# Optimization experiments

Measured on AMD Instinct MI355X. Metric: run time of the kernel, lower is better.

Reference implementation:

```python
import jax, jax.numpy as jnp
import numpy as np
from jax import lax

B = 2
IMG = 640.0
MIN_LEVEL, MAX_LEVEL = 3, 7
NUM_CLASSES = 91          # includes background (index 0)
MAX_TOTAL = 100
IOU_THR = 0.3
SCORE_THR = 0.05
PRE_NMS = 5000
BBOX_CLIP = float(np.log(1000.0 / 16.0))  # standard box-transform clip


def _level_anchors(level):
    """RetinaNet-style anchors for one pyramid level, [H*W*9, 4] in (y1,x1,y2,x2)."""
    stride = 2 ** level
    feat = int(IMG) // stride
    cy = (np.arange(feat, dtype=np.float32) + 0.5) * stride
    cx = (np.arange(feat, dtype=np.float32) + 0.5) * stride
    cy, cx = np.meshgrid(cy, cx, indexing='ij')
    base = 4.0 * stride
    anchors = []
    for octave in (2 ** 0.0, 2 ** (1.0 / 3.0), 2 ** (2.0 / 3.0)):
        for ar in (0.5, 1.0, 2.0):
            h = base * octave * np.sqrt(ar)
            w = base * octave / np.sqrt(ar)
            anchors.append(np.stack([cy - h / 2, cx - w / 2, cy + h / 2, cx + w / 2], -1))
    a = np.stack(anchors, -2).reshape(-1, 4)
    return a.astype(np.float32)


def setup_inputs():
    key = jax.random.key(0)
    inp = {}
    for level in range(MIN_LEVEL, MAX_LEVEL + 1):
        anc = _level_anchors(level)
        n = anc.shape[0]
        key, kb, kc = jax.random.split(key, 3)
        inp[f'box_outputs_{level}'] = 0.2 * jax.random.normal(kb, (B, n, 4), jnp.float32)
        inp[f'class_outputs_{level}'] = jax.random.normal(kc, (B, n, NUM_CLASSES), jnp.float32) - 2.0
        inp[f'anchor_boxes_{level}'] = jnp.broadcast_to(jnp.asarray(anc)[None], (B, n, 4))
    inp['image_shape'] = jnp.full((B, 2), IMG, jnp.float32)
    return inp


def _decode_boxes(enc, anchors):
    # faithful to box_utils.decode_boxes (with the +1/-1 pixel convention)
    dy, dx = enc[..., 0], enc[..., 1]
    dh = jnp.minimum(enc[..., 2], BBOX_CLIP)
    dw = jnp.minimum(enc[..., 3], BBOX_CLIP)
    ah = anchors[..., 2] - anchors[..., 0] + 1.0
    aw = anchors[..., 3] - anchors[..., 1] + 1.0
    ayc = anchors[..., 0] + 0.5 * ah
    axc = anchors[..., 1] + 0.5 * aw
    yc = dy * ah + ayc
    xc = dx * aw + axc
    h = jnp.exp(dh) * ah
    w = jnp.exp(dw) * aw
    ymin = yc - 0.5 * h
    xmin = xc - 0.5 * w
    return jnp.stack([ymin, xmin, ymin + h - 1.0, xmin + w - 1.0], axis=-1)


def _clip_boxes(boxes, image_shape):
    h = image_shape[:, 0:1]
    w = image_shape[:, 1:2]
    max_len = jnp.stack([h, w, h, w], axis=-1)  # [B,1,4]
    return jnp.clip(boxes, 0.0, max_len)


def _greedy_nms(scores, boxes):
    """Sorted greedy NMS over one (batch, class) lane.
    scores: [K] sorted descending (filtered entries are -1), boxes: [K,4].
    Returns top MAX_TOTAL selected (score, box) in descending score order,
    padded with score=-1 / zero boxes (matches sorted_non_max_suppression_padded).
    """
    areas = (boxes[:, 2] - boxes[:, 0]) * (boxes[:, 3] - boxes[:, 1])

    def step(active, _):
        masked = jnp.where(active, scores, -jnp.inf)
        i = jnp.argmax(masked)
        s = masked[i]
        valid = s > -1.0
        b = boxes[i]
        yy1 = jnp.maximum(b[0], boxes[:, 0])
        xx1 = jnp.maximum(b[1], boxes[:, 1])
        yy2 = jnp.minimum(b[2], boxes[:, 2])
        xx2 = jnp.minimum(b[3], boxes[:, 3])
        inter = jnp.maximum(yy2 - yy1, 0.0) * jnp.maximum(xx2 - xx1, 0.0)
        iou = inter / ((b[2] - b[0]) * (b[3] - b[1]) + areas - inter + 1e-8)
        active = active & (iou <= IOU_THR)
        active = active.at[i].set(False)
        out_s = jnp.where(valid, s, -1.0)
        out_b = jnp.where(valid, b, jnp.zeros_like(b))
        return active, (out_s, out_b)

    _, (sel_s, sel_b) = lax.scan(step, jnp.ones(scores.shape[0], bool), None, length=MAX_TOTAL)
    return sel_s, sel_b


def reference(box_outputs_3, box_outputs_4, box_outputs_5, box_outputs_6, box_outputs_7,
              class_outputs_3, class_outputs_4, class_outputs_5, class_outputs_6, class_outputs_7,
              anchor_boxes_3, anchor_boxes_4, anchor_boxes_5, anchor_boxes_6, anchor_boxes_7,
              image_shape):
    box_list = [box_outputs_3, box_outputs_4, box_outputs_5, box_outputs_6, box_outputs_7]
    cls_list = [class_outputs_3, class_outputs_4, class_outputs_5, class_outputs_6, class_outputs_7]
    anc_list = [anchor_boxes_3, anchor_boxes_4, anchor_boxes_5, anchor_boxes_6, anchor_boxes_7]

    boxes, scores = [], []
    for bo, co, an in zip(box_list, cls_list, anc_list):
        scores.append(jax.nn.sigmoid(co)[..., 1:])            # drop background class 0
        boxes.append(_clip_boxes(_decode_boxes(bo, an), image_shape))
    boxes = jnp.concatenate(boxes, axis=1)                     # [B,N,4] class-agnostic
    scores = jnp.concatenate(scores, axis=1)                   # [B,N,C]

    scores_t = jnp.transpose(scores, (0, 2, 1))                # [B,C,N]
    k = min(scores_t.shape[-1], PRE_NMS)
    top_s, idx = lax.top_k(scores_t, k)                        # [B,C,K]
    top_b = jax.vmap(lambda b, i: b[i])(boxes, idx)            # [B,C,K,4]

    # filter_boxes_by_scores: score -> -1, boxes -> 0 below threshold
    mask = top_s >= SCORE_THR
    top_s = jnp.where(mask, top_s, -1.0)
    top_b = top_b * mask[..., None].astype(top_b.dtype)

    sel_s, sel_b = jax.vmap(jax.vmap(_greedy_nms))(top_s, top_b)  # [B,C,T], [B,C,T,4]
    Bsz, C, T = sel_s.shape
    classes = jnp.broadcast_to(jnp.arange(C, dtype=jnp.int32)[None, :, None], (Bsz, C, T))

    flat_s = sel_s.reshape(Bsz, C * T)
    flat_b = sel_b.reshape(Bsz, C * T, 4)
    flat_c = classes.reshape(Bsz, C * T)

    final_s, fidx = lax.top_k(flat_s, MAX_TOTAL)
    final_b = jnp.take_along_axis(flat_b, fidx[..., None], axis=1)
    final_c = jnp.take_along_axis(flat_c, fidx, axis=1) + 1    # nmsed_classes += 1
    valid = jnp.sum((final_s > -1.0).astype(jnp.int32), axis=1)
    return final_b, final_s, final_c, valid
```

## Files before the change

kernel.cpp:

```cpp
#include <hip/hip_runtime.h>
#include <hip/hip_bf16.h>

typedef unsigned long long u64;
typedef unsigned int u32;

#define A_TOTAL 76725
#define NCLS 90
#define KTOP 5000u
#define MAXT 100
#define KTHR 0x3D4CCCCDu
#define TCAP 2048u
#define SCAP 512u
#define NSEL 384u

__device__ __forceinline__ u64 pack_key(u32 k, u32 i) {
  return ((u64)k << 32) | (u64)(0xFFFFFFFFu - i);
}

__device__ __forceinline__ int dig05(u64 k) {
  float s = __uint_as_float((u32)(k >> 32));
  int d = (int)((s - 0.5f) * 8175.0f);
  return min(max(d, 0), 4095);
}

__device__ __forceinline__ void cut4096w(const u32* hh, u32 need, int wl,
                                         u32& B, u32& incl, u32& above, u32& total) {
  int lo = wl << 6;
  u32 s = 0;
  #pragma unroll
  for (int j = 0; j < 64; ++j) s += hh[lo + j];
  u32 suf = s;
  #pragma unroll
  for (int off = 1; off < 64; off <<= 1) {
    u32 v = __shfl_down(suf, off, 64);
    if (wl < 64 - off) suf += v;
  }
  total = __shfl(suf, 0, 64);
  if (total < need) { B = 0; incl = total; above = 0; return; }
  u32 sufnext = suf - s;
  bool cross = (suf >= need) && (sufnext < need);
  u64 bal = __ballot(cross);
  int gl = (int)__ffsll((unsigned long long)bal) - 1;
  int glo = gl << 6;
  u32 aboveG = __shfl(sufnext, gl, 64);
  u32 hb = hh[glo + wl];
  u32 sufb = hb;
  #pragma unroll
  for (int off = 1; off < 64; off <<= 1) {
    u32 v = __shfl_down(sufb, off, 64);
    if (wl < 64 - off) sufb += v;
  }
  bool c2 = (aboveG + sufb >= need) && (aboveG + sufb - hb < need);
  u64 bal2 = __ballot(c2);
  int jB = (int)__ffsll((unsigned long long)bal2) - 1;
  B = (u32)(glo + jB);
  incl = aboveG + __shfl(sufb, jB, 64);
  above = incl - __shfl(hb, jB, 64);
}

__device__ __forceinline__ void bitonic_desc(u64* a, u32 n, int tid, int nth) {
  u32 P = 2; while (P < n) P <<= 1;
  for (u32 i = tid; i < P; i += nth) if (i >= n) a[i] = 0ULL;
  __syncthreads();
  for (u32 kk = 2; kk <= P; kk <<= 1) {
    for (u32 jj = kk >> 1; jj; jj >>= 1) {
      for (u32 i = tid; i < P; i += nth) {
        u32 ixj = i ^ jj;
        if (ixj > i) {
          u64 x = a[i], y = a[ixj];
          bool up = ((i & kk) == 0);
          if (up ? (x < y) : (x > y)) { a[i] = y; a[ixj] = x; }
        }
      }
      __syncthreads();
    }
  }
}

__device__ __forceinline__ int bitset_scan(const u64* key_s, const float4* boxes4, size_t bbase,
                                           int C, float4* wbox, float4* bbox,
                                           float* outS, float* outB, int w, int wl) {
  int cur = 0;
  while (w < MAXT && cur < C) {
    int p = cur + wl;
    bool valid = (p < C);
    u64 kk = valid ? key_s[p] : 0ull;
    float4 mybox = make_float4(-3e30f, -3e30f, -3e30f, -3e30f);
    if (valid) {
      u32 idx = 0xFFFFFFFFu - (u32)(kk & 0xFFFFFFFFull);
      mybox = boxes4[bbase + idx];
    }
    bbox[wl] = mybox;
    float myarea = (mybox.z - mybox.x) * (mybox.w - mybox.y);
    bool alive = valid;
    for (int j = 0; j < w; ++j) {
      float4 pb = wbox[j];
      float yy1 = fmaxf(pb.x, mybox.x), xx1 = fmaxf(pb.y, mybox.y);
      float yy2 = fminf(pb.z, mybox.z), xx2 = fminf(pb.w, mybox.w);
      float inter = fmaxf(yy2 - yy1, 0.0f) * fmaxf(xx2 - xx1, 0.0f);
      bool bad = false;
      if (inter > 0.0f) {
        float pa = (pb.z - pb.x) * (pb.w - pb.y);
        bad = inter / (pa + myarea - inter + 1e-8f) > 0.3f;
      }
      alive = alive && !bad;
    }
    u64 krow = 0ull;
    int jmax = C - cur; if (jmax > 64) jmax = 64;
    for (int j = 0; j < jmax; ++j) {
      float4 pb = bbox[j];
      float yy1 = fmaxf(pb.x, mybox.x), xx1 = fmaxf(pb.y, mybox.y);
      float yy2 = fminf(pb.z, mybox.z), xx2 = fminf(pb.w, mybox.w);
      float inter = fmaxf(yy2 - yy1, 0.0f) * fmaxf(xx2 - xx1, 0.0f);
      bool kill = false;
      if (inter > 0.0f) {
        float pa = (pb.z - pb.x) * (pb.w - pb.y);
        kill = inter / (pa + myarea - inter + 1e-8f) > 0.3f;
      }
      if (kill) krow |= (1ull << j);
    }
    u32 krlo = (u32)krow, krhi = (u32)(krow >> 32);
    u64 amask = __ballot(alive);
    int myord = -1;
    while (amask != 0ull && w < MAXT) {
      int js = (int)__ffsll((unsigned long long)amask) - 1;
      u32 klo = __shfl(krlo, js, 64);
      u32 khi = __shfl(krhi, js, 64);
      u64 kr = ((u64)khi << 32) | (u64)klo;
      if (wl == js) myord = w;
      amask &= ~kr;
      amask &= ~(1ull << js);
      w++;
    }
    if (myord >= 0) {
      outS[myord] = __uint_as_float((u32)(kk >> 32));
      *(float4*)(outB + myord * 4) = mybox;
      wbox[myord] = mybox;
    }
    cur += 64;
  }
  return w;
}

__device__ __forceinline__ int lazy_scan_g(const u64* key_s, const float4* boxes4, size_t bbase,
                                           int C, float4* wbox, float* outS, float* outB,
                                           int w, int wl) {
  int cur = 0;
  while (w < MAXT && cur < C) {
    int p = cur + wl;
    bool alive = (p < C);
    u64 kk = alive ? key_s[p] : 0ull;
    float4 mybox = make_float4(0.f, 0.f, 0.f, 0.f);
    if (alive) {
      u32 idx = 0xFFFFFFFFu - (u32)(kk & 0xFFFFFFFFull);
      mybox = boxes4[bbase + idx];
    }
    float myarea = (mybox.z - mybox.x) * (mybox.w - mybox.y);
    for (int j = 0; j < w; ++j) {
      float4 pb = wbox[j];
      float yy1 = fmaxf(pb.x, mybox.x), xx1 = fmaxf(pb.y, mybox.y);
      float yy2 = fminf(pb.z, mybox.z), xx2 = fminf(pb.w, mybox.w);
      float inter = fmaxf(yy2 - yy1, 0.0f) * fmaxf(xx2 - xx1, 0.0f);
      bool bad = false;
      if (inter > 0.0f) {
        float pa = (pb.z - pb.x) * (pb.w - pb.y);
        bad = inter / (pa + myarea - inter + 1e-8f) > 0.3f;
      }
      alive = alive && !bad;
    }
    for (;;) {
      u64 bal = __ballot(alive);
      if (bal == 0ull) break;
      int js = (int)__ffsll((unsigned long long)bal) - 1;
      float4 pb;
      pb.x = __shfl(mybox.x, js, 64);
      pb.y = __shfl(mybox.y, js, 64);
      pb.z = __shfl(mybox.z, js, 64);
      pb.w = __shfl(mybox.w, js, 64);
      u64 wk = __shfl(kk, js, 64);
      if (wl == 0) {
        outS[w] = __uint_as_float((u32)(wk >> 32));
        *(float4*)(outB + w * 4) = pb;
        wbox[w] = pb;
      }
      w++;
      if (w >= MAXT) break;
      if (wl <= js) alive = false;
      else if (alive) {
        float yy1 = fmaxf(pb.x, mybox.x), xx1 = fmaxf(pb.y, mybox.y);
        float yy2 = fminf(pb.z, mybox.z), xx2 = fminf(pb.w, mybox.w);
        float inter = fmaxf(yy2 - yy1, 0.0f) * fmaxf(xx2 - xx1, 0.0f);
        if (inter > 0.0f) {
          float pa = (pb.z - pb.x) * (pb.w - pb.y);
          if (inter / (pa + myarea - inter + 1e-8f) > 0.3f) alive = false;
        }
      }
    }
    cur += 64;
  }
  return w;
}

__global__ __launch_bounds__(256) void zero_kernel(u32* __restrict__ p, int n) {
  int i = blockIdx.x * 256 + threadIdx.x;
  if (i < n) p[i] = 0;
}

__device__ __forceinline__ void coll_elem(int i, float x, int b, int base, int slice,
                                          u64* __restrict__ listT_g, u32* __restrict__ cnt_pad) {
  if (x >= 0.0f) {
    u32 a = (u32)i / 91u;
    u32 c = (u32)i - a * 91u;
    if (c != 0u) {
      float s = 1.0f / (1.0f + expf(-x));
      int lane = b * NCLS + (int)c - 1;
      u32 idx = (u32)base + a;
      u32 p = atomicAdd(&cnt_pad[lane * 128 + slice * 16], 1u);
      if (p < SCAP) listT_g[(((size_t)lane * 8 + slice) << 9) + p] = pack_key(__float_as_uint(s), idx);
    }
  }
}

__global__ __launch_bounds__(256) void front_kernel(
    const float* __restrict__ bx0, const float* __restrict__ bx1, const float* __restrict__ bx2,
    const float* __restrict__ bx3, const float* __restrict__ bx4,
    const float* __restrict__ an0, const float* __restrict__ an1, const float* __restrict__ an2,
    const float* __restrict__ an3, const float* __restrict__ an4,
    const float* __restrict__ c3, const float* __restrict__ c4, const float* __restrict__ c5,
    const float* __restrict__ c6, const float* __restrict__ c7,
    const float* __restrict__ img, float* __restrict__ boxes,
    u64* __restrict__ listT_g, u32* __restrict__ cnt_pad)
{
  int blk = blockIdx.x, tid = threadIdx.x;
  if (blk < 600) {
    int t = blk * 256 + tid;
    if (t >= 2 * A_TOTAL) return;
    int b = t / A_TOTAL, a = t % A_TOTAL;
    const float* bp; const float* ap; int al; int nl;
    if (a < 57600)      { bp = bx0; ap = an0; al = a;          nl = 57600; }
    else if (a < 72000) { bp = bx1; ap = an1; al = a - 57600;  nl = 14400; }
    else if (a < 75600) { bp = bx2; ap = an2; al = a - 72000;  nl = 3600;  }
    else if (a < 76500) { bp = bx3; ap = an3; al = a - 75600;  nl = 900;   }
    else                { bp = bx4; ap = an4; al = a - 76500;  nl = 225;   }
    float4 e  = *(const float4*)(bp + ((size_t)b * nl + al) * 4);
    float4 an = *(const float4*)(ap + ((size_t)b * nl + al) * 4);
    const float CLIP = 4.135166556742356f;
    float ah  = an.z - an.x + 1.0f;
    float aw  = an.w - an.y + 1.0f;
    float ayc = an.x + 0.5f * ah;
    float axc = an.y + 0.5f * aw;
    float dh = fminf(e.z, CLIP), dw = fminf(e.w, CLIP);
    float yc = e.x * ah + ayc;
    float xc = e.y * aw + axc;
    float h  = expf(dh) * ah;
    float w  = expf(dw) * aw;
    float ymin = yc - 0.5f * h;
    float xmin = xc - 0.5f * w;
    float ymax = ymin + h - 1.0f;
    float xmax = xmin + w - 1.0f;
    float H = img[b * 2 + 0], W = img[b * 2 + 1];
    float4 o;
    o.x = fminf(fmaxf(ymin, 0.0f), H);
    o.y = fminf(fmaxf(xmin, 0.0f), W);
    o.z = fminf(fmaxf(ymax, 0.0f), H);
    o.w = fminf(fmaxf(xmax, 0.0f), W);
    *(float4*)(boxes + (size_t)t * 4) = o;
    return;
  }
  int blk2 = blk - 600;
  int slice = blk2 & 7;
  const float* cls; int n, base, b, loc, J, lvl;
  if (blk2 < 2560)      { lvl = 0; cls = c3; n = 57600; base = 0;     J = 1280; int r = blk2;        b = r >= J; loc = b ? r - J : r; }
  else if (blk2 < 3200) { lvl = 1; cls = c4; n = 14400; base = 57600; J = 320;  int r = blk2 - 2560; b = r >= J; loc = b ? r - J : r; }
  else if (blk2 < 3360) { lvl = 2; cls = c5; n = 3600;  base = 72000; J = 80;   int r = blk2 - 3200; b = r >= J; loc = b ? r - J : r; }
  else if (blk2 < 3400) { lvl = 3; cls = c6; n = 900;   base = 75600; J = 20;   int r = blk2 - 3360; b = r >= J; loc = b ? r - J : r; }
  else                  { lvl = 4; cls = c7; n = 225;   base = 76500; J = 10;   int r = blk2 - 3400; b = r >= J; loc = b ? r - J : r; }

  if (lvl <= 3) {
    int F4 = n * 91 / 4;
    int chunk = (F4 + J - 1) / J;
    int q0 = loc * chunk;
    int q1 = q0 + chunk; if (q1 > F4) q1 = F4;
    const float4* src4 = (const float4*)(cls + (size_t)b * n * 91);
    for (int q = q0 + tid; q < q1; q += 256) {
      float4 v = src4[q];
      int i0 = q << 2;
      coll_elem(i0,     v.x, b, base, slice, listT_g, cnt_pad);
      coll_elem(i0 + 1, v.y, b, base, slice, listT_g, cnt_pad);
      coll_elem(i0 + 2, v.z, b, base, slice, listT_g, cnt_pad);
      coll_elem(i0 + 3, v.w, b, base, slice, listT_g, cnt_pad);
    }
  } else {
    int F = n * 91;
    int chunk = (F + J - 1) / J;
    int s0 = loc * chunk;
    int s1 = s0 + chunk; if (s1 > F) s1 = F;
    const float* src = cls + (size_t)b * F;
    for (int i = s0 + tid; i < s1; i += 256) coll_elem(i, src[i], b, base, slice, listT_g, cnt_pad);
  }
}

__global__ __launch_bounds__(256) void nms_kernel(
    const float* __restrict__ c3, const float* __restrict__ c4, const float* __restrict__ c5,
    const float* __restrict__ c6, const float* __restrict__ c7,
    const float* __restrict__ boxes, const u64* __restrict__ listT_g,
    const u32* __restrict__ cnt_pad, float* __restrict__ nms_s, float* __restrict__ nms_b)
{
  __shared__ __align__(16) char big[40960];
  __shared__ __align__(16) u64 listE[2048];
  __shared__ u64 key_s[2048];
  __shared__ __align__(16) u32 histL[4096];
  __shared__ float4 wbox[MAXT];
  __shared__ float4 bbox[64];
  __shared__ u32 wtot[4];
  __shared__ u32 sh_flag, sh_mid, sh_bigS, sh_cS;
  __shared__ u64 sh_minPrev;
  __shared__ u32 sh_w, sh_done, sh_eidx, sh_Rthr, sh_eSorted, sh_bigF;
  __shared__ u32 sh_B, sh_incl, sh_above, sh_total, sh_cA, sh_cE, sh_B2;

  int tid = threadIdx.x;
  int lane = blockIdx.x;
  int b = lane / NCLS, c = lane % NCLS;
  const float4* boxes4 = (const float4*)boxes;
  size_t bbase = (size_t)b * A_TOTAL;
  const u64 thrpack = ((u64)KTHR) << 32;

  float* outS = nms_s + (size_t)lane * MAXT;
  float* outB = nms_b + (size_t)lane * MAXT * 4;

  u32 pre[9]; pre[0] = 0;
  bool of = false;
  #pragma unroll
  for (int j = 0; j < 8; ++j) {
    u32 cj = cnt_pad[lane * 128 + j * 16];
    of |= (cj > SCAP);
    pre[j + 1] = pre[j] + cj;
  }
  u32 cnt = pre[8];
  if (tid == 0) { sh_flag = (of || cnt > TCAP) ? 1u : 0u; sh_mid = 0; sh_bigS = 0; }
  __syncthreads();

  if (!sh_flag) {
    u64 kr[8];
    #pragma unroll
    for (int r = 0; r < 8; ++r) {
      u32 s = (u32)tid + (u32)r * 256u;
      u64 k = 0ull;
      if (s < cnt) {
        u32 j = 0;
        #pragma unroll
        for (int t = 1; t < 8; ++t) if (s >= pre[t]) j = (u32)t;
        k = listT_g[(((size_t)lane * 8 + j) << 9) + (s - pre[j])];
      }
      kr[r] = k;
    }

    for (int i = tid; i < 4096; i += 256) histL[i] = 0;
    __syncthreads();
    #pragma unroll
    for (int r = 0; r < 8; ++r) if (kr[r]) atomicAdd(&histL[dig05(kr[r])], 1u);
    __syncthreads();
    if (tid < 64) {
      u32 Bx, ix, ax, tx;
      cut4096w(histL, NSEL, tid, Bx, ix, ax, tx);
      if (tid == 0) { sh_B = Bx; sh_incl = ix; sh_total = tx; sh_cS = 0; }
    }
    __syncthreads();
    u32 B = sh_B, incl = sh_incl, total = sh_total;
    bool selAll = (total < NSEL);
    u32 Csel = selAll ? total : incl;
    if (Csel <= 768u) {
      u64* sel = (u64*)histL;
      #pragma unroll
      for (int r = 0; r < 8; ++r) {
        u64 k = kr[r];
        if (k && (selAll || (u32)dig05(k) >= B)) {
          u32 p = atomicAdd(&sh_cS, 1u);
          if (p < 768u) sel[p] = k;
        }
      }
      __syncthreads();
      u32 Cs = sh_cS; if (Cs > 768u) Cs = 768u;
      for (u32 j = tid; j < Cs; j += 256) {
        u64 kj = sel[j];
        u32 rk = 0;
        for (u32 i2 = 0; i2 < Cs; ++i2) rk += (sel[i2] > kj) ? 1u : 0u;
        key_s[rk] = kj;
      }
      __syncthreads();
      if (tid < 64) {
        int w = bitset_scan(key_s, boxes4, bbase, (int)Cs, wbox, bbox, outS, outB, 0, tid);
        if (tid == 0) {
          sh_w = (u32)w;
          if (w < MAXT) { if (selAll) sh_flag = 1; else sh_mid = 1; }
        }
      }
    } else {
      if (tid == 0) sh_mid = 1;
    }
    __syncthreads();

    if (sh_mid && !sh_flag) {
      for (int i = tid; i < 4096; i += 256) histL[i] = 0;
      if (tid == 0) sh_bigS = 0;
      __syncthreads();
      #pragma unroll
      for (int r = 0; r < 8; ++r) if (kr[r]) atomicAdd(&histL[dig05(kr[r])], 1u);
      __syncthreads();
      {
        int t0 = tid << 4;
        u32 hloc[16]; u32 ssum = 0;
        #pragma unroll
        for (int j = 0; j < 16; ++j) { hloc[j] = histL[t0 + j]; ssum += hloc[j]; }
        int wl = tid & 63, wid = tid >> 6;
        u32 suf = ssum;
        #pragma unroll
        for (int off = 1; off < 64; off <<= 1) {
          u32 v = __shfl_down(suf, off, 64);
          if (wl < 64 - off) suf += v;
        }
        if (wl == 0) wtot[wid] = suf;
        __syncthreads();
        u32 cross = 0;
        for (int w2 = wid + 1; w2 < 4; ++w2) cross += wtot[w2];
        u32 run = (suf - ssum) + cross;
        #pragma unroll
        for (int j = 15; j >= 0; --j) { u32 b2 = run; run += hloc[j]; histL[t0 + j] = b2; }
      }
      __syncthreads();
      #pragma unroll
      for (int r = 0; r < 8; ++r) {
        u64 k = kr[r];
        if (k) {
          u32 pos = atomicAdd(&histL[dig05(k)], 1u);
          if (pos < TCAP) key_s[pos] = k;
        }
      }
      __syncthreads();
      {
        int t0 = tid << 4;
        for (int j = 0; j < 16; ++j) {
          u32 d = (u32)(t0 + j);
          u32 end = histL[d];
          u32 start = (d == 4095u) ? 0u : histL[d + 1];
          u32 cc = end - start;
          if (cc >= 2u) {
            if (cc <= 48u) {
              for (u32 a2 = start + 1; a2 < end; ++a2) {
                u64 kv = key_s[a2];
                int bi = (int)a2 - 1;
                while (bi >= (int)start && key_s[bi] < kv) { key_s[bi + 1] = key_s[bi]; --bi; }
                key_s[bi + 1] = kv;
              }
            } else sh_bigS = 1;
          }
        }
      }
      __syncthreads();
      if (sh_bigS) bitonic_desc(key_s, cnt, tid, 256);
      if (tid < 64) {
        int w = bitset_scan(key_s, boxes4, bbase, (int)cnt, wbox, bbox, outS, outB, 0, tid);
        if (tid == 0) {
          sh_w = (u32)w;
          if (w < MAXT) sh_flag = 1;
        }
      }
    }
  }
  __syncthreads();
  if (!sh_flag) {
    u32 w = sh_w;
    for (u32 p = w + (u32)tid; p < MAXT; p += 256) {
      outS[p] = -1.0f;
      *(float4*)(outB + p * 4) = make_float4(0.f, 0.f, 0.f, 0.f);
    }
    return;
  }

  auto sb_of = [&](int i) -> u32 {
    const float* p; int al, nl;
    if (i < 57600)      { p = c3; al = i;          nl = 57600; }
    else if (i < 72000) { p = c4; al = i - 57600;  nl = 14400; }
    else if (i < 75600) { p = c5; al = i - 72000;  nl = 3600;  }
    else if (i < 76500) { p = c6; al = i - 75600;  nl = 900;   }
    else                { p = c7; al = i - 76500;  nl = 225;   }
    float x = p[((size_t)b * nl + al) * 91 + (c + 1)];
    float s = 1.0f / (1.0f + expf(-x));
    return __float_as_uint(s);
  };

  u64* listA = (u64*)big;
  for (int i = tid; i < 4096; i += 256) histL[i] = 0;
  if (tid == 0) {
    sh_cA = 0; sh_cE = 0; sh_w = 0; sh_done = 0; sh_eidx = 0; sh_eSorted = 0; sh_minPrev = ~0ull;
  }
  __syncthreads();
  for (int i = tid; i < A_TOTAL; i += 256) atomicAdd(&histL[sb_of(i) >> 19], 1u);
  __syncthreads();
  if (tid < 64) {
    u32 Bx, ix, ax, tx;
    cut4096w(histL, KTOP, tid, Bx, ix, ax, tx);
    if (tid == 0) sh_B = Bx;
  }
  __syncthreads();
  u32 B = sh_B;
  for (int i = tid; i < A_TOTAL; i += 256) {
    u32 u = sb_of(i);
    u32 bkt = u >> 19;
    if (bkt > B) {
      u32 p = atomicAdd(&sh_cA, 1u);
      if (p < 5120u) listA[p] = pack_key(u, (u32)i);
    } else if (bkt == B) {
      u32 p = atomicAdd(&sh_cE, 1u);
      if (p < 2048u) listE[p] = pack_key(u, (u32)i);
    }
  }
  __syncthreads();
  u32 g = sh_cA, h = sh_cE;
  if (h > 2048u) {
    for (int i = tid; i < 4096; i += 256) histL[i] = 0;
    if (tid == 0) sh_cE = 0;
    __syncthreads();
    for (int i = tid; i < A_TOTAL; i += 256) {
      u32 u = sb_of(i);
      if ((u >> 19) == B) atomicAdd(&histL[(u >> 7) & 0xFFFu], 1u);
    }
    __syncthreads();
    u32 R1 = KTOP - g;
    if (tid < 64) {
      u32 Bx, ix, ax, tx;
      cut4096w(histL, R1, tid, Bx, ix, ax, tx);
      if (tid == 0) sh_B2 = Bx;
    }
    __syncthreads();
    u32 B2 = sh_B2;
    for (int i = tid; i < A_TOTAL; i += 256) {
      u32 u = sb_of(i);
      if ((u >> 19) == B) {
        u32 sb2 = (u >> 7) & 0xFFFu;
        if (sb2 > B2) {
          u32 p = atomicAdd(&sh_cA, 1u);
          if (p < 5120u) listA[p] = pack_key(u, (u32)i);
        } else if (sb2 == B2) {
          u32 p = atomicAdd(&sh_cE, 1u);
          if (p < 2048u) listE[p] = pack_key(u, (u32)i);
        }
      }
    }
    __syncthreads();
    g = sh_cA; h = sh_cE; if (h > 2048u) h = 2048u;
  }
  if (g > 5120u) g = 5120u;
  u32 R = (g < KTOP) ? (KTOP - g) : 0u; if (R > h) R = h;

  u64 ak[20];
  #pragma unroll
  for (int r = 0; r < 20; ++r) {
    u32 s2 = (u32)tid + (u32)r * 256u;
    u64 kp = (s2 < g) ? listA[s2] : 0ull;
    if (kp < thrpack) kp = 0ull;
    ak[r] = kp;
  }
  __syncthreads();
  u32* cntArr = (u32*)big;

  const float LO0  = 0.04f;
  const float INV0 = 4096.0f / (1.001f - 0.04f);

  for (int seg = 0; seg < 7200; ++seg) {
    __syncthreads();
    if (sh_w >= MAXT || sh_done) break;
    u64 minPrev = sh_minPrev;

    int digLvl = 0;
    u32 A_B0 = 0, A_B1 = 0;
    float lo1 = 0.f, inv1 = 0.f;
    u64 kMask = 0, kPref = 0;
    int m1shift = 32;
    int selMode = -1;
    u32 selB = 0;
    u32 C = 0;
    bool fromE = false;

    for (int lvl = 0; lvl < 8; ++lvl) {
      for (int i = tid; i < 4096; i += 256) histL[i] = 0;
      __syncthreads();
      #pragma unroll
      for (int r = 0; r < 20; ++r) {
        u64 k = ak[r];
        if (!k || k >= minPrev) continue;
        float s = __uint_as_float((u32)(k >> 32));
        if (digLvl >= 1) { int d0 = (int)((s - LO0) * INV0); d0 = min(max(d0, 0), 4095); if ((u32)d0 != A_B0) continue; }
        if (digLvl >= 2) { int d1 = (int)((s - lo1) * inv1); d1 = min(max(d1, 0), 4095); if ((u32)d1 != A_B1) continue; }
        if (digLvl >= 3 && ((k & kMask) != kPref)) continue;
        u32 d;
        if (digLvl == 0)      { int t0 = (int)((s - LO0) * INV0); d = (u32)min(max(t0, 0), 4095); }
        else if (digLvl == 1) { int t1 = (int)((s - lo1) * inv1); d = (u32)min(max(t1, 0), 4095); }
        else                  d = (u32)((k >> m1shift) & 0xFFFull);
        atomicAdd(&histL[d], 1u);
      }
      __syncthreads();
      if (tid < 64) {
        u32 Bx, ix, ax, tx;
        cut4096w(histL, 1024u, tid, Bx, ix, ax, tx);
        if (tid == 0) { sh_B = Bx; sh_incl = ix; sh_above = ax; sh_total = tx; }
      }
      __syncthreads();
      u32 total = sh_total, incl = sh_incl, above = sh_above, Bx = sh_B;
      if (total == 0u)   { fromE = true; break; }
      if (total < 1024u) { selMode = 0; C = total; break; }
      if (incl <= 2048u) { selMode = 1; selB = Bx; C = incl; break; }
      if (above > 0u)    { selMode = 2; selB = Bx; C = above; break; }
      if (digLvl == 0) {
        A_B0 = Bx;
        lo1 = LO0 + (float)Bx / INV0;
        inv1 = INV0 * 4096.0f;
        digLvl = 1;
      } else if (digLvl == 1) {
        A_B1 = Bx;
        digLvl = 2; m1shift = 32;
      } else {
        kPref |= ((u64)Bx << m1shift);
        kMask |= (0xFFFull << m1shift);
        m1shift -= 12;
        digLvl++;
      }
      __syncthreads();
    }

    if (fromE) {
      if (!sh_eSorted) {
        bitonic_desc(listE, h, tid, 256);
        if (tid == 0) {
          u32 lo = 0, hi2 = h;
          while (lo < hi2) { u32 mid = (lo + hi2) >> 1; if (listE[mid] >= thrpack) lo = mid + 1; else hi2 = mid; }
          sh_Rthr = (R < lo) ? R : lo;
          sh_eSorted = 1;
        }
        __syncthreads();
      }
      u32 eidx = sh_eidx;
      u32 take = (sh_Rthr > eidx) ? (sh_Rthr - eidx) : 0u;
      if (take > 2048u) take = 2048u;
      if (take == 0u) { if (tid == 0) sh_done = 1; continue; }
      for (u32 i = tid; i < take; i += 256) key_s[i] = listE[eidx + i];
      C = take;
      if (tid == 0) sh_eidx = eidx + take;
    } else {
      u32 hloc[16];
      {
        int t0 = tid << 4;
        u32 ssum = 0;
        #pragma unroll
        for (int j = 0; j < 16; ++j) { hloc[j] = histL[t0 + j]; ssum += hloc[j]; }
        int wl = tid & 63, wid = tid >> 6;
        u32 suf = ssum;
        #pragma unroll
        for (int off = 1; off < 64; off <<= 1) {
          u32 v = __shfl_down(suf, off, 64);
          if (wl < 64 - off) suf += v;
        }
        if (wl == 0) wtot[wid] = suf;
        __syncthreads();
        u32 cross = 0;
        for (int w2 = wid + 1; w2 < 4; ++w2) cross += wtot[w2];
        u32 run = (suf - ssum) + cross;
        #pragma unroll
        for (int j = 15; j >= 0; --j) { u32 base2 = run; run += hloc[j]; histL[t0 + j] = base2; }
      }
      for (int i = tid; i < 4096; i += 256) cntArr[i] = 0;
      if (tid == 0) sh_bigF = 0;
      __syncthreads();
      #pragma unroll
      for (int r = 0; r < 20; ++r) {
        u64 k = ak[r];
        if (!k || k >= minPrev) continue;
        float s = __uint_as_float((u32)(k >> 32));
        if (digLvl >= 1) { int d0 = (int)((s - LO0) * INV0); d0 = min(max(d0, 0), 4095); if ((u32)d0 != A_B0) continue; }
        if (digLvl >= 2) { int d1 = (int)((s - lo1) * inv1); d1 = min(max(d1, 0), 4095); if ((u32)d1 != A_B1) continue; }
        if (digLvl >= 3 && ((k & kMask) != kPref)) continue;
        u32 d;
        if (digLvl == 0)      { int t0x = (int)((s - LO0) * INV0); d = (u32)min(max(t0x, 0), 4095); }
        else if (digLvl == 1) { int t1x = (int)((s - lo1) * inv1); d = (u32)min(max(t1x, 0), 4095); }
        else                  d = (u32)((k >> m1shift) & 0xFFFull);
        if (selMode == 1)      { if (d < selB) continue; }
        else if (selMode == 2) { if (d <= selB) continue; }
        u32 pos = histL[d] + atomicAdd(&cntArr[d], 1u);
        if (pos < 2048u) key_s[pos] = k;
      }
      __syncthreads();
      {
        int t0 = tid << 4;
        for (int j = 0; j < 16; ++j) {
          u32 bkt = (u32)(t0 + j);
          u32 cc = cntArr[bkt];
          if (cc >= 2u) {
            if (cc <= 48u) {
              u32 basep = histL[bkt];
              for (u32 a2 = 1; a2 < cc; ++a2) {
                u64 kv = key_s[basep + a2];
                int bi = (int)a2 - 1;
                while (bi >= 0 && key_s[basep + bi] < kv) { key_s[basep + bi + 1] = key_s[basep + bi]; --bi; }
                key_s[basep + bi + 1] = kv;
              }
            } else sh_bigF = 1;
          }
        }
      }
      __syncthreads();
      if (sh_bigF) bitonic_desc(key_s, C, tid, 256);
      if (tid == 0) sh_minPrev = key_s[C - 1];
    }
    __syncthreads();

    if (tid < 64) {
      int w = lazy_scan_g(key_s, boxes4, bbase, (int)C, wbox, outS, outB, (int)sh_w, tid);
      if (tid == 0) sh_w = (u32)w;
    }
  }

  __syncthreads();
  u32 w = sh_w;
  for (u32 p = w + (u32)tid; p < MAXT; p += 256) {
    outS[p] = -1.0f;
    *(float4*)(outB + p * 4) = make_float4(0.f, 0.f, 0.f, 0.f);
  }
}

__global__ __launch_bounds__(256) void merge_kernel(
    const float* __restrict__ nms_s, const float* __restrict__ nms_b,
    float* __restrict__ out_b, float* __restrict__ out_s,
    float* __restrict__ out_c, float* __restrict__ out_v)
{
  __shared__ u64 keys[NCLS * MAXT];
  __shared__ u32 hist[4096];
  __shared__ u64 sel[640];
  __shared__ u32 sh_cnt, sh_valid;
  __shared__ u32 sh_B, sh_incl, sh_above, sh_total;

  int b = blockIdx.x, tid = threadIdx.x;
  const int NTOT = NCLS * MAXT;

  for (int i = tid; i < NTOT; i += 256) {
    float s = nms_s[(size_t)b * NTOT + i];
    u32 u = __float_as_uint(s);
    u = (u & 0x80000000u) ? ~u : (u | 0x80000000u);
    keys[i] = ((u64)u << 32) | (u64)(0xFFFFFFFFu - (u32)i);
  }
  if (tid == 0) { sh_cnt = 0; sh_valid = 0; }

  u64 prefVal = 0;
  u64 T = 0;
  u32 need = MAXT;
  const int shifts[6] = {52, 40, 28, 16, 4, 0};
  const int widths[6] = {12, 12, 12, 12, 12, 4};
  for (int lvl = 0; lvl < 6; ++lvl) {
    int s = shifts[lvl], w = widths[lvl];
    for (int i = tid; i < 4096; i += 256) hist[i] = 0;
    __syncthreads();
    u32 dmask = (1u << w) - 1u;
    for (int i = tid; i < NTOT; i += 256) {
      u64 k = keys[i];
      if (lvl > 0 && (k >> (s + w)) != (prefVal >> (s + w))) continue;
      atomicAdd(&hist[(u32)((k >> s) & dmask)], 1u);
    }
    __syncthreads();
    if (tid < 64) {
      u32 Bx, ix, ax, tx;
      cut4096w(hist, need, tid, Bx, ix, ax, tx);
      if (tid == 0) { sh_B = Bx; sh_incl = ix; sh_above = ax; sh_total = tx; }
    }
    __syncthreads();
    u32 B = sh_B, incl = sh_incl, above = sh_above;
    if (incl <= 512u || lvl == 5) {
      T = prefVal | ((u64)B << s);
      break;
    }
    prefVal |= ((u64)B << s);
    need -= above;
  }
  __syncthreads();

  for (int i = tid; i < NTOT; i += 256) {
    u64 k = keys[i];
    if (k >= T) {
      u32 p = atomicAdd(&sh_cnt, 1u);
      if (p < 640u) sel[p] = k;
    }
  }
  __syncthreads();
  u32 cnt = sh_cnt; if (cnt > 640u) cnt = 640u;

  for (u32 j = tid; j < cnt; j += 256) {
    u64 kj = sel[j];
    u32 r = 0;
    for (u32 i = 0; i < cnt; ++i) r += (sel[i] > kj) ? 1u : 0u;
    if (r < (u32)MAXT) {
      u32 u = (u32)(kj >> 32);
      u32 bits = (u & 0x80000000u) ? (u ^ 0x80000000u) : ~u;
      float sc = __uint_as_float(bits);
      u32 flat = 0xFFFFFFFFu - (u32)(kj & 0xFFFFFFFFull);
      int cls = (int)(flat / MAXT), pos = (int)(flat % MAXT);
      out_s[b * MAXT + r] = sc;
      out_c[b * MAXT + r] = (float)(cls + 1);
      *(float4*)(out_b + ((size_t)b * MAXT + r) * 4) =
          *(const float4*)(nms_b + (((size_t)b * NCLS + cls) * MAXT + pos) * 4);
      if (sc > -1.0f) atomicAdd(&sh_valid, 1u);
    }
  }
  __syncthreads();
  if (tid == 0) out_v[b] = (float)sh_valid;
}

extern "C" void kernel_launch(void* const* d_in, const int* in_sizes, int n_in,
                              void* d_out, int out_size, void* d_ws, size_t ws_size,
                              hipStream_t stream)
{
  const float* box[5]; const float* cls[5]; const float* anc[5];
  bool interleaved = (in_sizes[1] == 2 * 57600 * 91);
  if (interleaved) {
    for (int l = 0; l < 5; ++l) {
      box[l] = (const float*)d_in[3 * l + 0];
      cls[l] = (const float*)d_in[3 * l + 1];
      anc[l] = (const float*)d_in[3 * l + 2];
    }
  } else {
    for (int l = 0; l < 5; ++l) {
      box[l] = (const float*)d_in[l];
      cls[l] = (const float*)d_in[5 + l];
      anc[l] = (const float*)d_in[10 + l];
    }
  }
  const float* img = (const float*)d_in[15];

  float* ws = (float*)d_ws;
  float* boxes_ws = ws;
  u32*   cnt_pad  = (u32*)(boxes_ws + 613800);
  u64*   listT_g  = (u64*)(cnt_pad + 180 * 128);
  float* nms_s    = (float*)(listT_g + 180 * 8 * 512);
  float* nms_b    = nms_s + 18000;

  const int NZ = 180 * 128;
  zero_kernel<<<(NZ + 255) / 256, 256, 0, stream>>>(cnt_pad, NZ);

  front_kernel<<<4020, 256, 0, stream>>>(
      box[0], box[1], box[2], box[3], box[4],
      anc[0], anc[1], anc[2], anc[3], anc[4],
      cls[0], cls[1], cls[2], cls[3], cls[4],
      img, boxes_ws, listT_g, cnt_pad);

  nms_kernel<<<180, 256, 0, stream>>>(cls[0], cls[1], cls[2], cls[3], cls[4],
                                      boxes_ws, listT_g, cnt_pad, nms_s, nms_b);

  float* out_b = (float*)d_out;
  float* out_s = out_b + 800;
  float* out_c = out_s + 200;
  float* out_v = out_c + 200;
  merge_kernel<<<2, 256, 0, stream>>>(nms_s, nms_b, out_b, out_s, out_c, out_v);
}
```

Baseline: 117.9 us.

## Derive a global score lower bound from per-class top-8 NMS survivors to prune candidates

Adds two kernels. The first runs a tiny NMS over each class's top-8 keys. The second finds the 100th-largest survivor score per batch, which is a lower bound on the final top-100 threshold. The NMS kernel now keeps only keys at or above that bound, replacing the histogram cut and the mid-path radix/bitonic sort. If more than SELCAP keys remain, or on panic, it falls back to the generic path. This costs two extra launches, including a single-block serial kernel, plus global reads in exchange for much smaller per-class sorts.

```diff
diff --git a/kernel.cpp b/kernel.cpp
--- a/kernel.cpp
+++ b/kernel.cpp
@@ -11,16 +11,10 @@
 #define KTHR 0x3D4CCCCDu
 #define TCAP 2048u
 #define SCAP 512u
-#define NSEL 384u
+#define SELCAP 512u
 
 __device__ __forceinline__ u64 pack_key(u32 k, u32 i) {
   return ((u64)k << 32) | (u64)(0xFFFFFFFFu - i);
-}
-
-__device__ __forceinline__ int dig05(u64 k) {
-  float s = __uint_as_float((u32)(k >> 32));
-  int d = (int)((s - 0.5f) * 8175.0f);
-  return min(max(d, 0), 4095);
 }
 
 __device__ __forceinline__ void cut4096w(const u32* hh, u32 need, int wl,
@@ -300,11 +294,151 @@
   }
 }
 
+__global__ __launch_bounds__(256) void top8_kernel(
+    const u64* __restrict__ listT_g, const u32* __restrict__ cnt_pad,
+    const float* __restrict__ boxes, u32* __restrict__ win8, u32* __restrict__ w8cnt)
+{
+  __shared__ u64 wred[4];
+  __shared__ u64 sh_top;
+  __shared__ u64 topk[8];
+  __shared__ float4 tb[8];
+  int tid = threadIdx.x;
+  int lane = blockIdx.x;
+
+  u32 pre[9]; pre[0] = 0;
+  bool of = false;
+  #pragma unroll
+  for (int j = 0; j < 8; ++j) {
+    u32 cj = cnt_pad[lane * 128 + j * 16];
+    of |= (cj > SCAP);
+    pre[j + 1] = pre[j] + cj;
+  }
+  u32 cnt = pre[8];
+  if (of || cnt > TCAP) { if (tid == 0) w8cnt[lane] = 0xFFFFu; return; }
+
+  u64 kr[8];
+  #pragma unroll
+  for (int r = 0; r < 8; ++r) {
+    u32 s = (u32)tid + (u32)r * 256u;
+    u64 k = 0ull;
+    if (s < cnt) {
+      u32 j = 0;
+      #pragma unroll
+      for (int t = 1; t < 8; ++t) if (s >= pre[t]) j = (u32)t;
+      k = listT_g[(((size_t)lane * 8 + j) << 9) + (s - pre[j])];
+    }
+    kr[r] = k;
+  }
+
+  int nt = 0;
+  for (int it = 0; it < 8; ++it) {
+    u64 m = kr[0];
+    #pragma unroll
+    for (int r = 1; r < 8; ++r) if (kr[r] > m) m = kr[r];
+    #pragma unroll
+    for (int off = 1; off < 64; off <<= 1) {
+      u64 o = __shfl_xor(m, off);
+      if (o > m) m = o;
+    }
+    if ((tid & 63) == 0) wred[tid >> 6] = m;
+    __syncthreads();
+    if (tid == 0) {
+      u64 w = wred[0];
+      if (wred[1] > w) w = wred[1];
+      if (wred[2] > w) w = wred[2];
+      if (wred[3] > w) w = wred[3];
+      sh_top = w;
+      topk[it] = w;
+    }
+    __syncthreads();
+    u64 ch = sh_top;
+    if (ch == 0ull) break;
+    #pragma unroll
+    for (int r = 0; r < 8; ++r) if (kr[r] == ch) kr[r] = 0ull;
+    nt = it + 1;
+  }
+  __syncthreads();
+  const float4* boxes4 = (const float4*)boxes;
+  size_t bbase = (size_t)(lane / NCLS) * A_TOTAL;
+  if (tid < nt) {
+    u32 idx = 0xFFFFFFFFu - (u32)(topk[tid] & 0xFFFFFFFFull);
+    tb[tid] = boxes4[bbase + idx];
+  }
+  __syncthreads();
+  if (tid == 0) {
+    float4 abox[8];
+    int w8 = 0;
+    for (int i = 0; i < nt; ++i) {
+      float4 mb = tb[i];
+      float ma = (mb.z - mb.x) * (mb.w - mb.y);
+      bool alive = true;
+      for (int j = 0; j < w8; ++j) {
+        float4 pb = abox[j];
+        float yy1 = fmaxf(pb.x, mb.x), xx1 = fmaxf(pb.y, mb.y);
+        float yy2 = fminf(pb.z, mb.z), xx2 = fminf(pb.w, mb.w);
+        float inter = fmaxf(yy2 - yy1, 0.0f) * fmaxf(xx2 - xx1, 0.0f);
+        if (inter > 0.0f) {
+          float pa = (pb.z - pb.x) * (pb.w - pb.y);
+          if (inter / (pa + ma - inter + 1e-8f) > 0.3f) alive = false;
+        }
+      }
+      if (alive) {
+        win8[lane * 8 + w8] = (u32)(topk[i] >> 32);
+        abox[w8] = mb;
+        w8++;
+      }
+    }
+    w8cnt[lane] = (u32)w8;
+  }
+}
+
+__global__ __launch_bounds__(256) void tlb2_kernel(const u32* __restrict__ win8,
+                                                   const u32* __restrict__ w8cnt,
+                                                   u32* __restrict__ tparams)
+{
+  __shared__ u32 vals[720];
+  __shared__ u32 sh_T, sh_tot, sh_panic;
+  int t = threadIdx.x;
+  if (t == 0) sh_panic = 0;
+  __syncthreads();
+  for (int b = 0; b < 2; ++b) {
+    if (t == 0) { sh_T = 0xFFFFFFFFu; sh_tot = 0; }
+    __syncthreads();
+    u32 mycnt = 0;
+    for (int i = t; i < 720; i += 256) {
+      int ln = b * NCLS + i / 8;
+      u32 cc = w8cnt[ln];
+      u32 v = 0;
+      if (cc == 0xFFFFu) { sh_panic = 1; }
+      else if ((u32)(i & 7) < cc) { v = win8[ln * 8 + (i & 7)]; mycnt++; }
+      vals[i] = v;
+    }
+    atomicAdd(&sh_tot, mycnt);
+    __syncthreads();
+    for (int i = t; i < 720; i += 256) {
+      u32 v = vals[i];
+      if (v) {
+        u32 r = 0;
+        for (int j = 0; j < 720; ++j) r += (vals[j] > v) ? 1u : 0u;
+        if (r <= 99u) atomicMin(&sh_T, v);
+      }
+    }
+    __syncthreads();
+    if (t == 0) {
+      tparams[b] = sh_T;
+      if (sh_tot < 100u || sh_T == 0xFFFFFFFFu) sh_panic = 1;
+    }
+    __syncthreads();
+  }
+  if (t == 0) tparams[2] = sh_panic;
+}
+
 __global__ __launch_bounds__(256) void nms_kernel(
     const float* __restrict__ c3, const float* __restrict__ c4, const float* __restrict__ c5,
     const float* __restrict__ c6, const float* __restrict__ c7,
     const float* __restrict__ boxes, const u64* __restrict__ listT_g,
-    const u32* __restrict__ cnt_pad, float* __restrict__ nms_s, float* __restrict__ nms_b)
+    const u32* __restrict__ cnt_pad, const u32* __restrict__ tparams,
+    float* __restrict__ nms_s, float* __restrict__ nms_b)
 {
   __shared__ __align__(16) char big[40960];
   __shared__ __align__(16) u64 listE[2048];
@@ -313,7 +447,7 @@
   __shared__ float4 wbox[MAXT];
   __shared__ float4 bbox[64];
   __shared__ u32 wtot[4];
-  __shared__ u32 sh_flag, sh_mid, sh_bigS, sh_cS;
+  __shared__ u32 sh_flag, sh_cS;
   __shared__ u64 sh_minPrev;
   __shared__ u32 sh_w, sh_done, sh_eidx, sh_Rthr, sh_eSorted, sh_bigF;
   __shared__ u32 sh_B, sh_incl, sh_above, sh_total, sh_cA, sh_cE, sh_B2;
@@ -337,50 +471,32 @@
     pre[j + 1] = pre[j] + cj;
   }
   u32 cnt = pre[8];
-  if (tid == 0) { sh_flag = (of || cnt > TCAP) ? 1u : 0u; sh_mid = 0; sh_bigS = 0; }
+  u32 Tlb = tparams[b], panic = tparams[2];
+  if (tid == 0) { sh_flag = (of || cnt > TCAP || panic) ? 1u : 0u; sh_cS = 0; }
   __syncthreads();
 
   if (!sh_flag) {
-    u64 kr[8];
+    const u64 Tpack = ((u64)Tlb) << 32;
+    u64* sel = (u64*)histL;
     #pragma unroll
     for (int r = 0; r < 8; ++r) {
       u32 s = (u32)tid + (u32)r * 256u;
-      u64 k = 0ull;
       if (s < cnt) {
         u32 j = 0;
         #pragma unroll
         for (int t = 1; t < 8; ++t) if (s >= pre[t]) j = (u32)t;
-        k = listT_g[(((size_t)lane * 8 + j) << 9) + (s - pre[j])];
-      }
-      kr[r] = k;
-    }
-
-    for (int i = tid; i < 4096; i += 256) histL[i] = 0;
-    __syncthreads();
-    #pragma unroll
-    for (int r = 0; r < 8; ++r) if (kr[r]) atomicAdd(&histL[dig05(kr[r])], 1u);
-    __syncthreads();
-    if (tid < 64) {
-      u32 Bx, ix, ax, tx;
-      cut4096w(histL, NSEL, tid, Bx, ix, ax, tx);
-      if (tid == 0) { sh_B = Bx; sh_incl = ix; sh_total = tx; sh_cS = 0; }
-    }
-    __syncthreads();
-    u32 B = sh_B, incl = sh_incl, total = sh_total;
-    bool selAll = (total < NSEL);
-    u32 Csel = selAll ? total : incl;
-    if (Csel <= 768u) {
-      u64* sel = (u64*)histL;
-      #pragma unroll
-      for (int r = 0; r < 8; ++r) {
-        u64 k = kr[r];
-        if (k && (selAll || (u32)dig05(k) >= B)) {
+        u64 k = listT_g[(((size_t)lane * 8 + j) << 9) + (s - pre[j])];
+        if (k >= Tpack) {
           u32 p = atomicAdd(&sh_cS, 1u);
-          if (p < 768u) sel[p] = k;
+          if (p < SELCAP) sel[p] = k;
         }
       }
-      __syncthreads();
-      u32 Cs = sh_cS; if (Cs > 768u) Cs = 768u;
+    }
+    __syncthreads();
+    u32 Cs = sh_cS;
+    if (Cs > SELCAP) {
+      if (tid == 0) sh_flag = 1;
+    } else {
       for (u32 j = tid; j < Cs; j += 256) {
         u64 kj = sel[j];
         u32 rk = 0;
@@ -390,80 +506,7 @@
       __syncthreads();
       if (tid < 64) {
         int w = bitset_scan(key_s, boxes4, bbase, (int)Cs, wbox, bbox, outS, outB, 0, tid);
-        if (tid == 0) {
-          sh_w = (u32)w;
-          if (w < MAXT) { if (selAll) sh_flag = 1; else sh_mid = 1; }
-        }
-      }
-    } else {
-      if (tid == 0) sh_mid = 1;
-    }
-    __syncthreads();
-
-    if (sh_mid && !sh_flag) {
-      for (int i = tid; i < 4096; i += 256) histL[i] = 0;
-      if (tid == 0) sh_bigS = 0;
-      __syncthreads();
-      #pragma unroll
-      for (int r = 0; r < 8; ++r) if (kr[r]) atomicAdd(&histL[dig05(kr[r])], 1u);
-      __syncthreads();
-      {
-        int t0 = tid << 4;
-        u32 hloc[16]; u32 ssum = 0;
-        #pragma unroll
-        for (int j = 0; j < 16; ++j) { hloc[j] = histL[t0 + j]; ssum += hloc[j]; }
-        int wl = tid & 63, wid = tid >> 6;
-        u32 suf = ssum;
-        #pragma unroll
-        for (int off = 1; off < 64; off <<= 1) {
-          u32 v = __shfl_down(suf, off, 64);
-          if (wl < 64 - off) suf += v;
-        }
-        if (wl == 0) wtot[wid] = suf;
-        __syncthreads();
-        u32 cross = 0;
-        for (int w2 = wid + 1; w2 < 4; ++w2) cross += wtot[w2];
-        u32 run = (suf - ssum) + cross;
-        #pragma unroll
-        for (int j = 15; j >= 0; --j) { u32 b2 = run; run += hloc[j]; histL[t0 + j] = b2; }
-      }
-      __syncthreads();
-      #pragma unroll
-      for (int r = 0; r < 8; ++r) {
-        u64 k = kr[r];
-        if (k) {
-          u32 pos = atomicAdd(&histL[dig05(k)], 1u);
-          if (pos < TCAP) key_s[pos] = k;
-        }
-      }
-      __syncthreads();
-      {
-        int t0 = tid << 4;
-        for (int j = 0; j < 16; ++j) {
-          u32 d = (u32)(t0 + j);
-          u32 end = histL[d];
-          u32 start = (d == 4095u) ? 0u : histL[d + 1];
-          u32 cc = end - start;
-          if (cc >= 2u) {
-            if (cc <= 48u) {
-              for (u32 a2 = start + 1; a2 < end; ++a2) {
-                u64 kv = key_s[a2];
-                int bi = (int)a2 - 1;
-                while (bi >= (int)start && key_s[bi] < kv) { key_s[bi + 1] = key_s[bi]; --bi; }
-                key_s[bi + 1] = kv;
-              }
-            } else sh_bigS = 1;
-          }
-        }
-      }
-      __syncthreads();
-      if (sh_bigS) bitonic_desc(key_s, cnt, tid, 256);
-      if (tid < 64) {
-        int w = bitset_scan(key_s, boxes4, bbase, (int)cnt, wbox, bbox, outS, outB, 0, tid);
-        if (tid == 0) {
-          sh_w = (u32)w;
-          if (w < MAXT) sh_flag = 1;
-        }
+        if (tid == 0) sh_w = (u32)w;
       }
     }
   }
@@ -836,7 +879,10 @@
   float* ws = (float*)d_ws;
   float* boxes_ws = ws;
   u32*   cnt_pad  = (u32*)(boxes_ws + 613800);
-  u64*   listT_g  = (u64*)(cnt_pad + 180 * 128);
+  u32*   win8     = cnt_pad + 180 * 128;
+  u32*   w8cnt    = win8 + 180 * 8;
+  u32*   tparams  = w8cnt + 180;
+  u64*   listT_g  = (u64*)(tparams + 4);
   float* nms_s    = (float*)(listT_g + 180 * 8 * 512);
   float* nms_b    = nms_s + 18000;
 
@@ -849,8 +895,12 @@
       cls[0], cls[1], cls[2], cls[3], cls[4],
       img, boxes_ws, listT_g, cnt_pad);
 
+  top8_kernel<<<180, 256, 0, stream>>>(listT_g, cnt_pad, boxes_ws, win8, w8cnt);
+
+  tlb2_kernel<<<1, 256, 0, stream>>>(win8, w8cnt, tparams);
+
   nms_kernel<<<180, 256, 0, stream>>>(cls[0], cls[1], cls[2], cls[3], cls[4],
-                                      boxes_ws, listT_g, cnt_pad, nms_s, nms_b);
+                                      boxes_ws, listT_g, cnt_pad, tparams, nms_s, nms_b);
 
   float* out_b = (float*)d_out;
   float* out_s = out_b + 800;
```

Measured after the change: 127.6 us. 1.08x slower.
